# Kernel tuning notes

Hardware: AMD Instinct MI355X
Metric: run time of the kernel (lower is better)

Reference implementation:

```python
import jax, jax.numpy as jnp
import numpy as np

F_DIM = 64      # feature_size
N_NODES = 64    # node_num
T_LEN = 24      # seq_len
N_HEADS = 8
BATCH = 16
E = F_DIM * N_NODES          # embed_dim = 4096
HD = E // N_HEADS            # head dim = 512


def setup_inputs() -> dict:
    key = jax.random.key(0)
    ks = jax.random.split(key, 5)
    s = 0.02
    return {
        "x": jax.random.normal(ks[0], (BATCH, F_DIM, T_LEN, N_NODES), jnp.float32),
        "Wqkv": jax.random.normal(ks[1], (3 * E, E), jnp.float32) * s,
        "bqkv": jnp.zeros((3 * E,), jnp.float32),
        "Wo": jax.random.normal(ks[2], (E, E), jnp.float32) * s,
        "bo": jnp.zeros((E,), jnp.float32),
        "Wfc": jax.random.normal(ks[3], (F_DIM, F_DIM), jnp.float32) * s,
        "bfc": jnp.zeros((F_DIM,), jnp.float32),
    }


def reference(x, Wqkv, bqkv, Wo, bo, Wfc, bfc):
    # x: [B, F, T, N]. Teacher-forcing branch of the original forward.
    B, T = x.shape[0], T_LEN
    # tokens: permute(2,0,1,3).reshape(T,B,E) -> E index = f*N + n
    xt = jnp.transpose(x, (2, 0, 1, 3)).reshape(T, B, E)  # [T,B,E]
    # in_proj is per-token, so projecting the full sequence once equals
    # the original's per-prefix projections.
    qkv = xt @ Wqkv.T + bqkv                               # [T,B,3E]
    q, k, v = jnp.split(qkv, 3, axis=-1)
    q = q.reshape(T, B, N_HEADS, HD)
    k = k.reshape(T, B, N_HEADS, HD)
    v = v.reshape(T, B, N_HEADS, HD)
    scores = jnp.einsum('qbhd,kbhd->bhqk', q, k) / np.sqrt(HD).astype(x.dtype)
    # NOTE: the original passes a float tril(ones) mask, which torch ADDS to
    # the scores (adds 1.0 on the lower triangle, 0 above). Reproduce exactly.
    tril_add = jnp.tril(jnp.ones((T, T), x.dtype))
    base = scores + tril_add                               # [B,H,T,T]
    # prefix lengths L = t+1 for steps t = 0..T-2
    L = jnp.arange(1, T)                                   # [T-1]
    keymask = jnp.arange(T)[None, :] < L[:, None]          # [T-1, T]
    masked = jnp.where(keymask[:, None, None, None, :], base[None], -jnp.inf)
    w = jax.nn.softmax(masked, axis=-1)                    # [T-1,B,H,T,T]
    ctx = jnp.einsum('tbhqk,kbhd->tbqhd', w, v).reshape(T - 1, B, T, E)
    out = ctx @ Wo.T + bo                                  # [T-1,B,T,E]
    # adaptive avg pool over the L valid query positions of each prefix
    qm = keymask.astype(out.dtype)                         # q < L
    pooled = jnp.einsum('tbqe,tq->tbe', out, qm) / L[:, None, None].astype(out.dtype)
    # torch: [B,E] -> reshape(B*N, F) -> fc -> relu -> reshape(B, F, 1, N)
    pred = jax.nn.relu(pooled.reshape(T - 1, B * N_NODES, F_DIM) @ Wfc.T + bfc)
    preds = pred.reshape(T - 1, B, F_DIM, N_NODES)         # row-major, same as torch
    first = x[:, :, :1, :]                                 # [B,F,1,N]
    rest = jnp.transpose(preds, (1, 2, 0, 3))              # [B,F,T-1,N]
    return jnp.concatenate([first, rest], axis=2)          # [B,F,T,N]
```

## Files before the change

kernel.cpp:

```cpp
#include <hip/hip_runtime.h>
#include <math.h>

#define F_DIM 64
#define N_NODES 64
#define T_LEN 24
#define N_HEADS 8
#define BATCH 16
#define E_DIM 4096
#define HD 512
#define QKV_N 12288
#define MB 384
#define TS 23
#define MP 368
#define MPAD 384

typedef unsigned short ushort_t;
typedef short bf16x8 __attribute__((ext_vector_type(8)));
typedef float f32x4 __attribute__((ext_vector_type(4)));

__device__ inline ushort_t f2bf(float f) {
    return (ushort_t)((__float_as_uint(f) + 0x8000u) >> 16);
}

__device__ inline void async_load16(const ushort_t* g, ushort_t* lds) {
    __builtin_amdgcn_global_load_lds(
        (const __attribute__((address_space(1))) unsigned int*)g,
        (__attribute__((address_space(3))) unsigned int*)lds,
        16, 0, 0);
}

__global__ void k_transpose(const float* __restrict__ x, ushort_t* __restrict__ xt) {
    int m = blockIdx.x;
    int t = m >> 4, b = m & 15;
    const float* xb = x + (size_t)b * (F_DIM * T_LEN * N_NODES) + (size_t)t * N_NODES;
    ushort_t* row = xt + (size_t)m * E_DIM;
    for (int e = threadIdx.x; e < E_DIM; e += 256) {
        int f = e >> 6, n = e & 63;
        row[e] = f2bf(xb[(size_t)f * (T_LEN * N_NODES) + n]);
    }
}

__global__ __launch_bounds__(256) void k_gemm_mfma(
    const ushort_t* __restrict__ A, const float* __restrict__ B,
    float* __restrict__ P, int N, int K, int kc)
{
    __shared__ __align__(16) ushort_t As[128 * 32];
    __shared__ __align__(16) ushort_t Bs[128 * 32];
    const int tid  = threadIdx.x;
    const int wave = tid >> 6, lane = tid & 63;
    const int wm = wave >> 1, wn = wave & 1;
    const int lr = lane & 15, lq = lane >> 4;
    const int n0 = blockIdx.x * 128, m0 = blockIdx.y * 128;
    const int kz = blockIdx.z * kc;

    f32x4 acc[4][4];
    #pragma unroll
    for (int i = 0; i < 4; ++i)
        #pragma unroll
        for (int j = 0; j < 4; ++j)
            acc[i][j] = (f32x4){0.f, 0.f, 0.f, 0.f};

    const int jA0 = ((wave * 2 + 0) * 64 + lane) * 16;
    const int jA1 = ((wave * 2 + 1) * 64 + lane) * 16;
    const int rA0 = jA0 >> 6, kA0 = (jA0 & 63) >> 1;
    const int rA1 = jA1 >> 6, kA1 = (jA1 & 63) >> 1;
    const ushort_t* gA0 = A + (size_t)(m0 + rA0) * K + kA0;
    const ushort_t* gA1 = A + (size_t)(m0 + rA1) * K + kA1;
    ushort_t* lA0 = As + (wave * 2 + 0) * 512;
    ushort_t* lA1 = As + (wave * 2 + 1) * 512;

    for (int k0 = kz; k0 < kz + kc; k0 += 32) {
        async_load16(gA0 + k0, lA0);
        async_load16(gA1 + k0, lA1);
        #pragma unroll
        for (int s = 0; s < 4; ++s) {
            int e4  = tid + s * 256;
            int row = e4 >> 3;
            int kq  = (e4 & 7) * 4;
            const float4 v = *(const float4*)(B + (size_t)(n0 + row) * K + k0 + kq);
            unsigned int ux = __float_as_uint(v.x) + 0x8000u;
            unsigned int uy = __float_as_uint(v.y) + 0x8000u;
            unsigned int uz = __float_as_uint(v.z) + 0x8000u;
            unsigned int uw = __float_as_uint(v.w) + 0x8000u;
            unsigned int p0 = __builtin_amdgcn_perm(uy, ux, 0x07060302u);
            unsigned int p1 = __builtin_amdgcn_perm(uw, uz, 0x07060302u);
            *(uint2*)&Bs[row * 32 + kq] = make_uint2(p0, p1);
        }
        __syncthreads();
        bf16x8 af[4], bfr[4];
        #pragma unroll
        for (int i = 0; i < 4; ++i)
            af[i] = *(const bf16x8*)&As[(wm * 64 + i * 16 + lr) * 32 + lq * 8];
        #pragma unroll
        for (int j = 0; j < 4; ++j)
            bfr[j] = *(const bf16x8*)&Bs[(wn * 64 + j * 16 + lr) * 32 + lq * 8];
        #pragma unroll
        for (int i = 0; i < 4; ++i)
            #pragma unroll
            for (int j = 0; j < 4; ++j)
                acc[i][j] = __builtin_amdgcn_mfma_f32_16x16x32_bf16(af[i], bfr[j], acc[i][j], 0, 0, 0);
        __syncthreads();
    }

    float* Pz = P + (size_t)blockIdx.z * MPAD * N;
    #pragma unroll
    for (int i = 0; i < 4; ++i) {
        int mi = m0 + wm * 64 + i * 16 + lq * 4;
        #pragma unroll
        for (int r = 0; r < 4; ++r) {
            #pragma unroll
            for (int j = 0; j < 4; ++j) {
                int n = n0 + wn * 64 + j * 16 + lr;
                Pz[(size_t)(mi + r) * N + n] = acc[i][j][r];
            }
        }
    }
}

__global__ void k_reduce(const float* __restrict__ P, const float* __restrict__ bias,
                         float* __restrict__ C, int N, int S) {
    int idx = blockIdx.x * 256 + threadIdx.x;
    size_t e = (size_t)idx * 4;
    int n = (int)(e % N);
    float4 a = *(const float4*)(P + e);
    for (int s = 1; s < S; ++s) {
        const float4 b = *(const float4*)(P + (size_t)s * MPAD * N + e);
        a.x += b.x; a.y += b.y; a.z += b.z; a.w += b.w;
    }
    const float4 bb = *(const float4*)(bias + n);
    a.x += bb.x; a.y += bb.y; a.z += bb.z; a.w += bb.w;
    *(float4*)(C + e) = a;
}

__global__ void k_scores(const float* __restrict__ qkv, float* __restrict__ wbar) {
    int bh = blockIdx.x;
    int b = bh >> 3, h = bh & 7;
    __shared__ float ss[T_LEN][25];
    __shared__ float isv[T_LEN][25];
    int tid = threadIdx.x, wave = tid >> 6, lane = tid & 63;
    const float scale = 0.044194173824159216f;
    for (int p = wave; p < T_LEN * T_LEN; p += 8) {
        int qi = p / 24, ki = p - qi * 24;
        const float* qp = qkv + (size_t)(qi * BATCH + b) * QKV_N + h * HD + lane * 8;
        const float* kp = qkv + (size_t)(ki * BATCH + b) * QKV_N + E_DIM + h * HD + lane * 8;
        float4 a0 = *(const float4*)qp, a1 = *(const float4*)(qp + 4);
        float4 c0 = *(const float4*)kp, c1 = *(const float4*)(kp + 4);
        float s = a0.x * c0.x + a0.y * c0.y + a0.z * c0.z + a0.w * c0.w
                + a1.x * c1.x + a1.y * c1.y + a1.z * c1.z + a1.w * c1.w;
        #pragma unroll
        for (int off = 32; off > 0; off >>= 1) s += __shfl_xor(s, off);
        if (lane == 0) {
            s *= scale;
            if (ki <= qi) s += 1.f;
            ss[qi][ki] = s;
        }
    }
    __syncthreads();
    if (tid < T_LEN) {
        int q = tid;
        float M = -1e30f;
        for (int k = 0; k < T_LEN; ++k) M = fmaxf(M, ss[q][k]);
        float run = 0.f;
        for (int k = 0; k < T_LEN; ++k) {
            float e = __expf(ss[q][k] - M);
            ss[q][k] = e;
            run += e;
            isv[q][k] = 1.f / run;
        }
    }
    __syncthreads();
    for (int p = tid; p < TS * T_LEN; p += 512) {
        int t = p / 24, k = p - t * 24;
        float w = 0.f;
        if (k <= t) {
            float sum = 0.f;
            for (int q = 0; q <= t; ++q) sum += ss[q][k] * isv[q][t];
            w = sum / (float)(t + 1);
        }
        wbar[(size_t)((t * BATCH + b) * N_HEADS + h) * T_LEN + k] = w;
    }
}

__global__ void k_cbar(const float* __restrict__ qkv, const float* __restrict__ wbar,
                       ushort_t* __restrict__ cbar) {
    int bh = blockIdx.x;
    int b = bh >> 3, h = bh & 7;
    __shared__ float vs[T_LEN * HD];
    __shared__ float wb[TS * T_LEN];
    int tid = threadIdx.x;
    for (int i4 = tid; i4 < T_LEN * HD / 4; i4 += 256) {
        int t = i4 >> 7, d4 = i4 & 127;
        *(float4*)&vs[t * HD + d4 * 4] =
            *(const float4*)&qkv[(size_t)(t * BATCH + b) * QKV_N + 2 * E_DIM + h * HD + d4 * 4];
    }
    for (int i = tid; i < TS * T_LEN; i += 256)
        wb[i] = wbar[(size_t)(((i / 24) * BATCH + b) * N_HEADS + h) * T_LEN + (i % 24)];
    __syncthreads();
    for (int t = 0; t < TS; ++t) {
        for (int d = tid; d < HD; d += 256) {
            float acc = 0.f;
            #pragma unroll
            for (int k = 0; k < T_LEN; ++k) acc += wb[t * 24 + k] * vs[k * HD + d];
            cbar[(size_t)(t * BATCH + b) * E_DIM + h * HD + d] = f2bf(acc);
        }
    }
}

__global__ void k_final(const float* __restrict__ pooled, const float* __restrict__ Wfc,
                        const float* __restrict__ bfc, float* __restrict__ out) {
    int tb = blockIdx.x;
    int t = tb >> 4, b = tb & 15;
    __shared__ float ps[E_DIM];
    __shared__ float wf[64 * 65];
    __shared__ float bf[64];
    int tid = threadIdx.x;
    for (int i = tid; i < E_DIM; i += 256) ps[i] = pooled[(size_t)tb * E_DIM + i];
    for (int i = tid; i < 64 * 64; i += 256) wf[(i >> 6) * 65 + (i & 63)] = Wfc[i];
    if (tid < 64) bf[tid] = bfc[tid];
    __syncthreads();
    for (int p = tid; p < 4096; p += 256) {
        int f = p >> 6, n = p & 63;
        float acc = bf[n];
        #pragma unroll
        for (int g = 0; g < 64; ++g) acc += ps[f * 64 + g] * wf[n * 65 + g];
        out[(size_t)((b * 64 + f) * T_LEN + (t + 1)) * N_NODES + n] = fmaxf(acc, 0.f);
    }
}

__global__ void k_first(const float* __restrict__ x, float* __restrict__ out) {
    int idx = blockIdx.x * 256 + threadIdx.x;
    if (idx >= BATCH * F_DIM * N_NODES) return;
    int b = idx >> 12, f = (idx >> 6) & 63, n = idx & 63;
    size_t o = ((size_t)(b * 64 + f) * T_LEN) * 64 + n;
    out[o] = x[o];
}

extern "C" void kernel_launch(void* const* d_in, const int* in_sizes, int n_in,
                              void* d_out, int out_size, void* d_ws, size_t ws_size,
                              hipStream_t stream) {
    const float* x    = (const float*)d_in[0];
    const float* Wqkv = (const float*)d_in[1];
    const float* bqkv = (const float*)d_in[2];
    const float* Wo   = (const float*)d_in[3];
    const float* bo   = (const float*)d_in[4];
    const float* Wfc  = (const float*)d_in[5];
    const float* bfc  = (const float*)d_in[6];
    float* out = (float*)d_out;

    char* wsb = (char*)d_ws;
    ushort_t* xt   = (ushort_t*)wsb;
    float*    qkv  = (float*)(wsb + 3145728);
    float*    wbar = (float*)(wsb + 3145728 + 18874368);
    ushort_t* cbar = (ushort_t*)(wsb + 3145728 + 18874368 + 282624);
    float*  pooled = (float*)(wsb + 3145728 + 18874368 + 282624 + 3145728);
    size_t base    = 3145728 + 18874368 + 282624 + 3145728 + 6291456;
    float*  pbuf   = (float*)(wsb + base);

    const size_t pstride = (size_t)MPAD * QKV_N * 4;
    int S = 1;
    if (ws_size >= base + 4 * pstride) S = 4;
    else if (ws_size >= base + 2 * pstride) S = 2;
    int Swo = 2 * S;

    hipLaunchKernelGGL(k_transpose, dim3(MB), dim3(256), 0, stream, x, xt);

    hipLaunchKernelGGL(k_gemm_mfma, dim3(QKV_N / 128, 3, S), dim3(256), 0, stream,
                       xt, Wqkv, pbuf, QKV_N, E_DIM, E_DIM / S);
    hipLaunchKernelGGL(k_reduce, dim3(MPAD * QKV_N / 4 / 256), dim3(256), 0, stream,
                       pbuf, bqkv, qkv, QKV_N, S);

    hipLaunchKernelGGL(k_scores, dim3(BATCH * N_HEADS), dim3(512), 0, stream, qkv, wbar);
    hipLaunchKernelGGL(k_cbar, dim3(BATCH * N_HEADS), dim3(256), 0, stream, qkv, wbar, cbar);

    hipLaunchKernelGGL(k_gemm_mfma, dim3(E_DIM / 128, 3, Swo), dim3(256), 0, stream,
                       cbar, Wo, pbuf, E_DIM, E_DIM, E_DIM / Swo);
    hipLaunchKernelGGL(k_reduce, dim3(MPAD * E_DIM / 4 / 256), dim3(256), 0, stream,
                       pbuf, bo, pooled, E_DIM, Swo);

    hipLaunchKernelGGL(k_final, dim3(TS * BATCH), dim3(256), 0, stream, pooled, Wfc, bfc, out);
    hipLaunchKernelGGL(k_first, dim3((BATCH * F_DIM * N_NODES + 255) / 256), dim3(256), 0, stream, x, out);
}
```

Before: 559.5 us.

## Tile GEMM as full-M by 64-column blocks, fuse attention scores and context kernels

The MFMA GEMM now gives each block all 384 rows of A and 64 columns of B, so each fp32 weight row is read and converted to bf16 only once instead of three times across M tiles. The split-K factors change: 2 for the QKV projection and up to 8 for the output projection. The scores and cbar kernels are merged into one 512-thread kernel that keeps the softmax-averaged weights in LDS, which removes the wbar round trip through global memory and one launch. In exchange the GEMM block uses more LDS and accumulator registers, which may reduce occupancy, and the A tile is now reloaded by every column block.

New measurement: 539.6 us. -3.5%, faster.

```diff
diff --git a/kernel.cpp b/kernel.cpp
--- a/kernel.cpp
+++ b/kernel.cpp
@@ -44,36 +44,36 @@
     const ushort_t* __restrict__ A, const float* __restrict__ B,
     float* __restrict__ P, int N, int K, int kc)
 {
-    __shared__ __align__(16) ushort_t As[128 * 32];
-    __shared__ __align__(16) ushort_t Bs[128 * 32];
+    __shared__ __align__(16) ushort_t As[384 * 32];
+    __shared__ __align__(16) ushort_t Bs[64 * 32];
     const int tid  = threadIdx.x;
     const int wave = tid >> 6, lane = tid & 63;
-    const int wm = wave >> 1, wn = wave & 1;
     const int lr = lane & 15, lq = lane >> 4;
-    const int n0 = blockIdx.x * 128, m0 = blockIdx.y * 128;
+    const int n0 = blockIdx.x * 64;
     const int kz = blockIdx.z * kc;
 
-    f32x4 acc[4][4];
+    f32x4 acc[6][4];
     #pragma unroll
-    for (int i = 0; i < 4; ++i)
+    for (int i = 0; i < 6; ++i)
         #pragma unroll
         for (int j = 0; j < 4; ++j)
             acc[i][j] = (f32x4){0.f, 0.f, 0.f, 0.f};
 
-    const int jA0 = ((wave * 2 + 0) * 64 + lane) * 16;
-    const int jA1 = ((wave * 2 + 1) * 64 + lane) * 16;
-    const int rA0 = jA0 >> 6, kA0 = (jA0 & 63) >> 1;
-    const int rA1 = jA1 >> 6, kA1 = (jA1 & 63) >> 1;
-    const ushort_t* gA0 = A + (size_t)(m0 + rA0) * K + kA0;
-    const ushort_t* gA1 = A + (size_t)(m0 + rA1) * K + kA1;
-    ushort_t* lA0 = As + (wave * 2 + 0) * 512;
-    ushort_t* lA1 = As + (wave * 2 + 1) * 512;
+    const int rb = lane >> 2, kp = (lane & 3) * 8;
+    const ushort_t* gA[6];
+    ushort_t* lA[6];
+    #pragma unroll
+    for (int s = 0; s < 6; ++s) {
+        int r = (wave * 6 + s) * 16 + rb;
+        gA[s] = A + (size_t)r * K + kp;
+        lA[s] = As + (wave * 6 + s) * 512;
+    }
 
     for (int k0 = kz; k0 < kz + kc; k0 += 32) {
-        async_load16(gA0 + k0, lA0);
-        async_load16(gA1 + k0, lA1);
-        #pragma unroll
-        for (int s = 0; s < 4; ++s) {
+        #pragma unroll
+        for (int s = 0; s < 6; ++s) async_load16(gA[s] + k0, lA[s]);
+        #pragma unroll
+        for (int s = 0; s < 2; ++s) {
             int e4  = tid + s * 256;
             int row = e4 >> 3;
             int kq  = (e4 & 7) * 4;
@@ -87,15 +87,15 @@
             *(uint2*)&Bs[row * 32 + kq] = make_uint2(p0, p1);
         }
         __syncthreads();
-        bf16x8 af[4], bfr[4];
-        #pragma unroll
-        for (int i = 0; i < 4; ++i)
-            af[i] = *(const bf16x8*)&As[(wm * 64 + i * 16 + lr) * 32 + lq * 8];
+        bf16x8 af[6], bfr[4];
+        #pragma unroll
+        for (int i = 0; i < 6; ++i)
+            af[i] = *(const bf16x8*)&As[(wave * 96 + i * 16 + lr) * 32 + lq * 8];
         #pragma unroll
         for (int j = 0; j < 4; ++j)
-            bfr[j] = *(const bf16x8*)&Bs[(wn * 64 + j * 16 + lr) * 32 + lq * 8];
-        #pragma unroll
-        for (int i = 0; i < 4; ++i)
+            bfr[j] = *(const bf16x8*)&Bs[(j * 16 + lr) * 32 + lq * 8];
+        #pragma unroll
+        for (int i = 0; i < 6; ++i)
             #pragma unroll
             for (int j = 0; j < 4; ++j)
                 acc[i][j] = __builtin_amdgcn_mfma_f32_16x16x32_bf16(af[i], bfr[j], acc[i][j], 0, 0, 0);
@@ -104,15 +104,13 @@
 
     float* Pz = P + (size_t)blockIdx.z * MPAD * N;
     #pragma unroll
-    for (int i = 0; i < 4; ++i) {
-        int mi = m0 + wm * 64 + i * 16 + lq * 4;
+    for (int i = 0; i < 6; ++i) {
+        int m = wave * 96 + i * 16 + lq * 4;
         #pragma unroll
         for (int r = 0; r < 4; ++r) {
             #pragma unroll
-            for (int j = 0; j < 4; ++j) {
-                int n = n0 + wn * 64 + j * 16 + lr;
-                Pz[(size_t)(mi + r) * N + n] = acc[i][j][r];
-            }
+            for (int j = 0; j < 4; ++j)
+                Pz[(size_t)(m + r) * N + n0 + j * 16 + lr] = acc[i][j][r];
         }
     }
 }
@@ -132,12 +130,20 @@
     *(float4*)(C + e) = a;
 }
 
-__global__ void k_scores(const float* __restrict__ qkv, float* __restrict__ wbar) {
+__global__ __launch_bounds__(512) void k_attn(const float* __restrict__ qkv,
+                                              ushort_t* __restrict__ cbar) {
     int bh = blockIdx.x;
     int b = bh >> 3, h = bh & 7;
+    __shared__ float vs[T_LEN * HD];
     __shared__ float ss[T_LEN][25];
     __shared__ float isv[T_LEN][25];
+    __shared__ float wbs[TS * T_LEN];
     int tid = threadIdx.x, wave = tid >> 6, lane = tid & 63;
+    for (int i4 = tid; i4 < T_LEN * HD / 4; i4 += 512) {
+        int t = i4 >> 7, d4 = (i4 & 127) * 4;
+        *(float4*)&vs[t * HD + d4] =
+            *(const float4*)&qkv[(size_t)(t * BATCH + b) * QKV_N + 2 * E_DIM + h * HD + d4];
+    }
     const float scale = 0.044194173824159216f;
     for (int p = wave; p < T_LEN * T_LEN; p += 8) {
         int qi = p / 24, ki = p - qi * 24;
@@ -177,32 +183,15 @@
             for (int q = 0; q <= t; ++q) sum += ss[q][k] * isv[q][t];
             w = sum / (float)(t + 1);
         }
-        wbar[(size_t)((t * BATCH + b) * N_HEADS + h) * T_LEN + k] = w;
-    }
-}
-
-__global__ void k_cbar(const float* __restrict__ qkv, const float* __restrict__ wbar,
-                       ushort_t* __restrict__ cbar) {
-    int bh = blockIdx.x;
-    int b = bh >> 3, h = bh & 7;
-    __shared__ float vs[T_LEN * HD];
-    __shared__ float wb[TS * T_LEN];
-    int tid = threadIdx.x;
-    for (int i4 = tid; i4 < T_LEN * HD / 4; i4 += 256) {
-        int t = i4 >> 7, d4 = i4 & 127;
-        *(float4*)&vs[t * HD + d4 * 4] =
-            *(const float4*)&qkv[(size_t)(t * BATCH + b) * QKV_N + 2 * E_DIM + h * HD + d4 * 4];
-    }
-    for (int i = tid; i < TS * T_LEN; i += 256)
-        wb[i] = wbar[(size_t)(((i / 24) * BATCH + b) * N_HEADS + h) * T_LEN + (i % 24)];
-    __syncthreads();
+        wbs[p] = w;
+    }
+    __syncthreads();
+    int d = tid;
     for (int t = 0; t < TS; ++t) {
-        for (int d = tid; d < HD; d += 256) {
-            float acc = 0.f;
-            #pragma unroll
-            for (int k = 0; k < T_LEN; ++k) acc += wb[t * 24 + k] * vs[k * HD + d];
-            cbar[(size_t)(t * BATCH + b) * E_DIM + h * HD + d] = f2bf(acc);
-        }
+        float a = 0.f;
+        #pragma unroll
+        for (int k = 0; k < T_LEN; ++k) a += wbs[t * 24 + k] * vs[k * HD + d];
+        cbar[(size_t)(t * BATCH + b) * E_DIM + h * HD + d] = f2bf(a);
     }
 }
 
@@ -250,29 +239,26 @@
     char* wsb = (char*)d_ws;
     ushort_t* xt   = (ushort_t*)wsb;
     float*    qkv  = (float*)(wsb + 3145728);
-    float*    wbar = (float*)(wsb + 3145728 + 18874368);
-    ushort_t* cbar = (ushort_t*)(wsb + 3145728 + 18874368 + 282624);
-    float*  pooled = (float*)(wsb + 3145728 + 18874368 + 282624 + 3145728);
-    size_t base    = 3145728 + 18874368 + 282624 + 3145728 + 6291456;
+    ushort_t* cbar = (ushort_t*)(wsb + 3145728 + 18874368);
+    float*  pooled = (float*)(wsb + 3145728 + 18874368 + 3145728);
+    size_t base    = 3145728 + 18874368 + 3145728 + 6291456;
     float*  pbuf   = (float*)(wsb + base);
 
-    const size_t pstride = (size_t)MPAD * QKV_N * 4;
-    int S = 1;
-    if (ws_size >= base + 4 * pstride) S = 4;
-    else if (ws_size >= base + 2 * pstride) S = 2;
-    int Swo = 2 * S;
+    const size_t pq = (size_t)MPAD * QKV_N * 4;
+    const size_t po = (size_t)MPAD * E_DIM * 4;
+    int S = (ws_size >= base + 2 * pq) ? 2 : 1;
+    int Swo = (ws_size >= base + 8 * po) ? 8 : ((ws_size >= base + 4 * po) ? 4 : 1);
 
     hipLaunchKernelGGL(k_transpose, dim3(MB), dim3(256), 0, stream, x, xt);
 
-    hipLaunchKernelGGL(k_gemm_mfma, dim3(QKV_N / 128, 3, S), dim3(256), 0, stream,
+    hipLaunchKernelGGL(k_gemm_mfma, dim3(QKV_N / 64, 1, S), dim3(256), 0, stream,
                        xt, Wqkv, pbuf, QKV_N, E_DIM, E_DIM / S);
     hipLaunchKernelGGL(k_reduce, dim3(MPAD * QKV_N / 4 / 256), dim3(256), 0, stream,
                        pbuf, bqkv, qkv, QKV_N, S);
 
-    hipLaunchKernelGGL(k_scores, dim3(BATCH * N_HEADS), dim3(512), 0, stream, qkv, wbar);
-    hipLaunchKernelGGL(k_cbar, dim3(BATCH * N_HEADS), dim3(256), 0, stream, qkv, wbar, cbar);
-
-    hipLaunchKernelGGL(k_gemm_mfma, dim3(E_DIM / 128, 3, Swo), dim3(256), 0, stream,
+    hipLaunchKernelGGL(k_attn, dim3(BATCH * N_HEADS), dim3(512), 0, stream, qkv, cbar);
+
+    hipLaunchKernelGGL(k_gemm_mfma, dim3(E_DIM / 64, 1, Swo), dim3(256), 0, stream,
                        cbar, Wo, pbuf, E_DIM, E_DIM, E_DIM / Swo);
     hipLaunchKernelGGL(k_reduce, dim3(MPAD * E_DIM / 4 / 256), dim3(256), 0, stream,
                        pbuf, bo, pooled, E_DIM, Swo);
```
